# Performance work log

Measured on AMD Instinct MI355X. Metric: run time of the kernel, lower is better.

Reference implementation:

```python
import jax, jax.numpy as jnp
import numpy as np

BS, NA, NE, NAL = 512, 10, 11, 9
H, HEADS, EDIM, ADIM, OWN, NACT, HYP = 64, 4, 8, 8, 14, 17, 64
EOUT = ((EDIM + 1) * H + 1) * HEADS   # 2308: fc1 weights + fc2 attack weights + fc2 attack bias, per head
AOUT = ADIM * H * HEADS               # 2048: ally fc1 weights only (non-MMM map)


def setup_inputs() -> dict:
    key = jax.random.key(0)
    ks = jax.random.split(key, 28)
    N = BS * NA
    s = 0.05
    rn = lambda k, shp: jax.random.normal(k, shp, jnp.float32)
    d = {
        "own_feats": rn(ks[0], (N, OWN)),
        "enemy_feats": rn(ks[1], (N * NE, EDIM)),
        "ally_feats": rn(ks[2], (N * NAL, ADIM)),
        "hidden_state": rn(ks[3], (N, H)),
        "agent_indices": jax.random.randint(ks[4], (N,), 0, NA),
        "last_action_indices": jax.random.randint(ks[5], (N,), 0, NACT),
        "fc1_own_w": rn(ks[6], (H, OWN)) * s,
        "fc1_own_b": rn(ks[7], (H,)) * s,
        "agent_emb": rn(ks[8], (NA, H)) * s,
        "action_emb": rn(ks[9], (NACT, H)) * s,
        "he_w1": rn(ks[10], (HYP, EDIM)) * s,
        "he_b1": rn(ks[11], (HYP,)) * s,
        "he_w2": rn(ks[12], (EOUT, HYP)) * s,
        "he_b2": rn(ks[13], (EOUT,)) * s,
        "ha_w1": rn(ks[14], (HYP, ADIM)) * s,
        "ha_b1": rn(ks[15], (HYP,)) * s,
        "ha_w2": rn(ks[16], (AOUT, HYP)) * s,
        "ha_b2": rn(ks[17], (AOUT,)) * s,
        "merge_in_w": rn(ks[18], (1, HEADS, H)) * s,
        "gru_w_ih": rn(ks[19], (3 * H, H)) * s,
        "gru_w_hh": rn(ks[20], (3 * H, H)) * s,
        "gru_b_ih": rn(ks[21], (3 * H,)) * s,
        "gru_b_hh": rn(ks[22], (3 * H,)) * s,
        "fc2_w": rn(ks[23], (6, H)) * s,
        "fc2_b": rn(ks[24], (6,)) * s,
        "merge_out_w": rn(ks[25], (1, HEADS, 1)) * s,
        "bs": BS,
    }
    return d


def reference(own_feats, enemy_feats, ally_feats, hidden_state, agent_indices,
              last_action_indices, fc1_own_w, fc1_own_b, agent_emb, action_emb,
              he_w1, he_b1, he_w2, he_b2, ha_w1, ha_b1, ha_w2, ha_b2,
              merge_in_w, gru_w_ih, gru_w_hh, gru_b_ih, gru_b_hh,
              fc2_w, fc2_b, merge_out_w, bs):
    N = bs * NA
    cut = (H + 1) * HEADS  # tail of hyper_enemy_out: fc2 attack weights + bias

    # own embedding + id/action embeddings
    emb_own = own_feats @ fc1_own_w.T + fc1_own_b \
        + agent_emb[agent_indices] + action_emb[last_action_indices]

    # enemy hypernet -> per-enemy fc1 weights, then per-entity bmm, sum over enemies
    he_out = jax.nn.relu(enemy_feats @ he_w1.T + he_b1) @ he_w2.T + he_b2  # [N*NE, EOUT]
    fc1_w_e = he_out[:, :-cut].reshape(-1, EDIM, H * HEADS)
    emb_e = jnp.einsum('ne,neh->nh', enemy_feats, fc1_w_e)
    emb_e = emb_e.reshape(N, NE, HEADS, H).sum(axis=1)  # [N, HEADS, H]

    # ally hypernet -> per-ally fc1 weights
    ha_out = jax.nn.relu(ally_feats @ ha_w1.T + ha_b1) @ ha_w2.T + ha_b2  # [N*NAL, AOUT]
    fc1_w_a = ha_out.reshape(-1, ADIM, H * HEADS)
    emb_a = jnp.einsum('na,nah->nh', ally_feats, fc1_w_a)
    emb_a = emb_a.reshape(N, NAL, HEADS, H).sum(axis=1)

    # softmax-weighted multi-head merge + own embedding
    w_in = jax.nn.softmax(merge_in_w, axis=1)  # [1, HEADS, H]
    emb = emb_own + jnp.sum(w_in * (emb_e + emb_a), axis=1)
    x = jax.nn.relu(emb)

    # GRUCell (torch gate order: reset, update, new)
    h_in = hidden_state.reshape(-1, H)
    gi = x @ gru_w_ih.T + gru_b_ih
    gh = h_in @ gru_w_hh.T + gru_b_hh
    i_r, i_z, i_n = jnp.split(gi, 3, axis=1)
    h_r, h_z, h_n = jnp.split(gh, 3, axis=1)
    r = jax.nn.sigmoid(i_r + h_r)
    z = jax.nn.sigmoid(i_z + h_z)
    n = jnp.tanh(i_n + r * h_n)
    hh = (1.0 - z) * n + z * h_in  # [N, H]

    q_normal = (hh @ fc2_w.T + fc2_b).reshape(bs, NA, 6)

    # attack Q values from hypernet-generated fc2
    fc2_w_att = he_out[:, -cut:-HEADS].reshape(N, NE * HEADS, H)
    fc2_b_att = he_out[:, -HEADS:].reshape(N, NE * HEADS)
    q_att = jnp.einsum('nh,nkh->nk', hh, fc2_w_att) + fc2_b_att  # [N, NE*HEADS]
    q_atts = q_att.reshape(N * NE, HEADS, 1)
    w_out = jax.nn.softmax(merge_out_w, axis=1)  # [1, HEADS, 1]
    q_attack = jnp.sum(w_out * q_atts, axis=1).reshape(bs, NA, NE)

    q = jnp.concatenate([q_normal, q_attack], axis=-1)  # [bs, NA, 6+NE]
    return q
```

## Files before the change

### kernel.cpp

```cpp
#include <hip/hip_runtime.h>
#include <hip/hip_bf16.h>
#include <math.h>

#define BS_    512
#define NA_    10
#define NE_    11
#define NAL_   9
#define H_     64
#define HEADS_ 4
#define EDIM_  8
#define ADIM_  8
#define OWN_   14
#define HYP_   64
#define NTOT_  (BS_*NA_)
#define AGB_   8

#define WGRU_US   67584
#define WVV_US    100352
#define WFC2_US   104448
#define WB_OFF    52736
#define B4_OFF    52800
#define FB_OFF    53056
#define WS_FLOATS 53072

typedef __attribute__((ext_vector_type(8))) short short8_t;
typedef __attribute__((ext_vector_type(4))) float f32x4;

__device__ __forceinline__ unsigned short to_bf16(float v) {
    unsigned u = __float_as_uint(v);
    u += 0x7fffu + ((u >> 16) & 1u);
    return (unsigned short)(u >> 16);
}
__device__ __forceinline__ unsigned pack2(float lo, float hi) {
    return ((unsigned)to_bf16(hi) << 16) | to_bf16(lo);
}

__global__ __launch_bounds__(256) void prep_kernel(
    const float* __restrict__ fc1_own_w, const float* __restrict__ fc1_own_b,
    const float* __restrict__ he_w2, const float* __restrict__ he_b2,
    const float* __restrict__ ha_w2, const float* __restrict__ ha_b2,
    const float* __restrict__ merge_in_w,
    const float* __restrict__ gru_w_ih, const float* __restrict__ gru_w_hh,
    const float* __restrict__ gru_b_ih, const float* __restrict__ gru_b_hh,
    const float* __restrict__ merge_out_w,
    const float* __restrict__ fc2_w, const float* __restrict__ fc2_b,
    float* __restrict__ ws)
{
    const int tid = blockIdx.x * blockDim.x + threadIdx.x;

    float wo0, wo1, wo2, wo3;
    {
        float e0 = expf(merge_out_w[0]), e1 = expf(merge_out_w[1]);
        float e2 = expf(merge_out_w[2]), e3 = expf(merge_out_w[3]);
        float inv = 1.0f / (e0 + e1 + e2 + e3);
        wo0 = e0*inv; wo1 = e1*inv; wo2 = e2*inv; wo3 = e3*inv;
    }

    if (tid < 65536) {
        const int half = tid >> 15;
        const int t    = tid & 32767;
        const int col  = t >> 9;
        const int idxL = t & 511;
        const int e    = idxL >> 6;
        const int kk   = idxL & 63;
        const float e0 = expf(merge_in_w[col]),       e1 = expf(merge_in_w[64 + col]);
        const float e2 = expf(merge_in_w[128 + col]), e3 = expf(merge_in_w[192 + col]);
        const float inv = 1.0f / (e0 + e1 + e2 + e3);
        const float wi[4] = { e0*inv, e1*inv, e2*inv, e3*inv };
        const float* Wsrc = half ? ha_w2 : he_w2;
        float v = 0.f;
#pragma unroll
        for (int hd = 0; hd < 4; hd++)
            v += wi[hd] * Wsrc[(size_t)(e*256 + hd*64 + col)*64 + kk];
        const int k   = half*512 + kk*8 + e;
        const int ks  = k >> 5, sub = k & 31;
        const int outp = (col >> 4)*16896 + ks*512 + (((sub >> 3) << 4) + (col & 15))*8 + (sub & 7);
        ((unsigned short*)ws)[outp] = to_bf16(v);
    } else if (tid < 67584) {
        const int t   = tid - 65536;
        const int col = t >> 5;
        const int io  = t & 31;
        float v = 0.f;
        if (io < 16) {
            const float e0 = expf(merge_in_w[col]),       e1 = expf(merge_in_w[64 + col]);
            const float e2 = expf(merge_in_w[128 + col]), e3 = expf(merge_in_w[192 + col]);
            const float inv = 1.0f / (e0 + e1 + e2 + e3);
            const float wi[4] = { e0*inv, e1*inv, e2*inv, e3*inv };
            const float* Bsrc = (io < 8) ? he_b2 : ha_b2;
            const int e = io & 7;
#pragma unroll
            for (int hd = 0; hd < 4; hd++)
                v += wi[hd] * Bsrc[e*256 + hd*64 + col];
        } else if (io < 30) {
            v = fc1_own_w[col*OWN_ + (io - 16)];
        } else if (io == 30) {
            v = fc1_own_b[col];
        }
        const int outp = (col >> 4)*16896 + 32*512 + (((io >> 3) << 4) + (col & 15))*8 + (io & 7);
        ((unsigned short*)ws)[outp] = to_bf16(v);
    } else if (tid < 100352) {
        const int t = tid - 67584;
        const int j  = t & 7;
        const int fl = (t >> 3) & 63;
        const int kstep = (t >> 9) & 3;
        const int T  = t >> 11;
        const int k  = kstep*32 + ((fl >> 4) << 3) + j;
        const int kk = k >> 1;
        const bool hside = (k & 1);
        const int c  = T*16 + (fl & 15);
        const int g  = c >> 6;
        const int u  = c & 63;
        float v;
        if (g == 0)      v = hside ? gru_w_hh[u*64 + kk]       : gru_w_ih[u*64 + kk];
        else if (g == 1) v = hside ? gru_w_hh[(64+u)*64 + kk]  : gru_w_ih[(64+u)*64 + kk];
        else if (g == 2) v = hside ? 0.f                        : gru_w_ih[(128+u)*64 + kk];
        else             v = hside ? gru_w_hh[(128+u)*64 + kk] : 0.f;
        ((unsigned short*)ws)[WGRU_US + t] = to_bf16(v);
    } else if (tid < 104448) {
        const int t = tid - 100352;
        const int j  = t & 7;
        const int fl = (t >> 3) & 63;
        const int kstep = (t >> 9) & 1;
        const int nt = t >> 10;
        const int k  = kstep*32 + ((fl >> 4) << 3) + j;
        const int col = nt*16 + (fl & 15);
        float v = wo0 * he_w2[(2048 + 0*64 + k)*64 + col]
                + wo1 * he_w2[(2048 + 1*64 + k)*64 + col]
                + wo2 * he_w2[(2048 + 2*64 + k)*64 + col]
                + wo3 * he_w2[(2048 + 3*64 + k)*64 + col];
        ((unsigned short*)ws)[WVV_US + t] = to_bf16(v);
    } else if (tid < 105472) {
        const int t = tid - 104448;
        const int j  = t & 7;
        const int fl = (t >> 3) & 63;
        const int kstep = t >> 9;
        const int k  = kstep*32 + ((fl >> 4) << 3) + j;
        const int col = fl & 15;
        float v = 0.f;
        if (col < 6)       v = fc2_w[col*64 + k];
        else if (col == 6) v = wo0*he_b2[2048 + 0*64 + k] + wo1*he_b2[2048 + 1*64 + k]
                             + wo2*he_b2[2048 + 2*64 + k] + wo3*he_b2[2048 + 3*64 + k];
        ((unsigned short*)ws)[WFC2_US + t] = to_bf16(v);
    } else if (tid < 105536) {
        const int k = tid - 105472;
        float v = wo0*he_w2[(2304+0)*64 + k] + wo1*he_w2[(2304+1)*64 + k]
                + wo2*he_w2[(2304+2)*64 + k] + wo3*he_w2[(2304+3)*64 + k];
        ws[WB_OFF + k] = v;
    } else if (tid < 105792) {
        const int c = tid - 105536;
        const int g = c >> 6, u = c & 63;
        float v;
        if (g == 0)      v = gru_b_ih[u]       + gru_b_hh[u];
        else if (g == 1) v = gru_b_ih[64 + u]  + gru_b_hh[64 + u];
        else if (g == 2) v = gru_b_ih[128 + u];
        else             v = gru_b_hh[128 + u];
        ws[B4_OFF + c] = v;
    } else if (tid < 105808) {
        const int col = tid - 105792;
        float v = 0.f;
        if (col < 6)       v = fc2_b[col];
        else if (col == 6) v = wo0*he_b2[2304] + wo1*he_b2[2305] + wo2*he_b2[2306] + wo3*he_b2[2307];
        ws[FB_OFF + col] = v;
    }
}

#define STG_ALLY 704
#define STG_HID  1280
#define STG_OWN  1792

#define AROW_ 1064

__global__ __launch_bounds__(512, 6) void main_kernel(
    const float* __restrict__ own_feats,
    const float* __restrict__ enemy_feats,
    const float* __restrict__ ally_feats,
    const float* __restrict__ hidden_state,
    const int*   __restrict__ agent_idx,
    const int*   __restrict__ last_act,
    const float* __restrict__ agent_emb,
    const float* __restrict__ action_emb,
    const float* __restrict__ he_w1,
    const float* __restrict__ he_b1,
    const float* __restrict__ ha_w1,
    const float* __restrict__ ha_b1,
    const float* __restrict__ ws,
    float* __restrict__ out)
{
    const int tid  = threadIdx.x;
    const int w    = tid >> 6;
    const int lane = tid & 63;
    const int n    = blockIdx.x * AGB_ + w;
    const int q    = w & 3;
    const int kh   = w >> 2;
    const unsigned short* ws_us = (const unsigned short*)ws;

    __shared__ __align__(16) unsigned short a_cmp[AGB_][AROW_];
    __shared__ __align__(16) float scratch[3104];
    float* const stg    = scratch;
    float* const GmF    = scratch;
    float* const pembMF = scratch + 2080;

    {
        const int n0 = blockIdx.x * AGB_;
        const float4* src = nullptr;
        float* dst = nullptr;
        if (tid < 176)      { src = (const float4*)(enemy_feats + (size_t)n0*88) + tid;         dst = stg + tid*4; }
        else if (tid < 320) { src = (const float4*)(ally_feats + (size_t)n0*72) + (tid-176);    dst = stg + STG_ALLY + (tid-176)*4; }
        else if (tid < 448) { src = (const float4*)(hidden_state + (size_t)n0*64) + (tid-320);  dst = stg + STG_HID + (tid-320)*4; }
        else if (tid < 476) { src = (const float4*)(own_feats + (size_t)n0*14) + (tid-448);     dst = stg + STG_OWN + (tid-448)*4; }
        if (src) *(float4*)dst = *src;
    }
    __syncthreads();

    float h_e[NE_];
    float embo, hin_reg;
    {
        const float4 w1a  = *(const float4*)(he_w1 + lane*8);
        const float4 w1b  = *(const float4*)(he_w1 + lane*8 + 4);
        const float  hb1  = he_b1[lane];
        const float* se = stg + w*88;

        float ps[8] = {0,0,0,0,0,0,0,0};
#pragma unroll
        for (int ei = 0; ei < NE_; ei++) {
            const float4 e0 = *(const float4*)(se + ei*8);
            const float4 e1 = *(const float4*)(se + ei*8 + 4);
            float h = hb1;
            h = fmaf(e0.x, w1a.x, h); h = fmaf(e0.y, w1a.y, h);
            h = fmaf(e0.z, w1a.z, h); h = fmaf(e0.w, w1a.w, h);
            h = fmaf(e1.x, w1b.x, h); h = fmaf(e1.y, w1b.y, h);
            h = fmaf(e1.z, w1b.z, h); h = fmaf(e1.w, w1b.w, h);
            h = fmaxf(h, 0.f);
            h_e[ei] = h;
            ps[0] = fmaf(e0.x, h, ps[0]); ps[1] = fmaf(e0.y, h, ps[1]);
            ps[2] = fmaf(e0.z, h, ps[2]); ps[3] = fmaf(e0.w, h, ps[3]);
            ps[4] = fmaf(e1.x, h, ps[4]); ps[5] = fmaf(e1.y, h, ps[5]);
            ps[6] = fmaf(e1.z, h, ps[6]); ps[7] = fmaf(e1.w, h, ps[7]);
        }
        {
            uint4 pk;
            pk.x = pack2(ps[0], ps[1]); pk.y = pack2(ps[2], ps[3]);
            pk.z = pack2(ps[4], ps[5]); pk.w = pack2(ps[6], ps[7]);
            *(uint4*)&a_cmp[w][lane*8] = pk;
        }

        const float4 wa1a = *(const float4*)(ha_w1 + lane*8);
        const float4 wa1b = *(const float4*)(ha_w1 + lane*8 + 4);
        const float  hba1 = ha_b1[lane];
        const float* sa = stg + STG_ALLY + w*72;
        float pa[8] = {0,0,0,0,0,0,0,0};
#pragma unroll
        for (int ai = 0; ai < NAL_; ai++) {
            const float4 a0 = *(const float4*)(sa + ai*8);
            const float4 a1 = *(const float4*)(sa + ai*8 + 4);
            float h = hba1;
            h = fmaf(a0.x, wa1a.x, h); h = fmaf(a0.y, wa1a.y, h);
            h = fmaf(a0.z, wa1a.z, h); h = fmaf(a0.w, wa1a.w, h);
            h = fmaf(a1.x, wa1b.x, h); h = fmaf(a1.y, wa1b.y, h);
            h = fmaf(a1.z, wa1b.z, h); h = fmaf(a1.w, wa1b.w, h);
            h = fmaxf(h, 0.f);
            pa[0] = fmaf(a0.x, h, pa[0]); pa[1] = fmaf(a0.y, h, pa[1]);
            pa[2] = fmaf(a0.z, h, pa[2]); pa[3] = fmaf(a0.w, h, pa[3]);
            pa[4] = fmaf(a1.x, h, pa[4]); pa[5] = fmaf(a1.y, h, pa[5]);
            pa[6] = fmaf(a1.z, h, pa[6]); pa[7] = fmaf(a1.w, h, pa[7]);
        }
        {
            uint4 pk;
            pk.x = pack2(pa[0], pa[1]); pk.y = pack2(pa[2], pa[3]);
            pk.z = pack2(pa[4], pa[5]); pk.w = pack2(pa[6], pa[7]);
            *(uint4*)&a_cmp[w][512 + lane*8] = pk;
        }

        if (lane < 8) {
            float s = 0.f;
            for (int ei = 0; ei < NE_; ei++) s += se[ei*8 + lane];
            a_cmp[w][1024 + lane] = to_bf16(s);
        } else if (lane < 16) {
            const int p = lane - 8;
            float s = 0.f;
            for (int ai = 0; ai < NAL_; ai++) s += sa[ai*8 + p];
            a_cmp[w][1032 + p] = to_bf16(s);
        } else if (lane < 32) {
            float v;
            if (lane < 30)       v = stg[STG_OWN + w*OWN_ + (lane - 16)];
            else if (lane == 30) v = 1.f;
            else                 v = 0.f;
            a_cmp[w][1024 + lane] = to_bf16(v);
        }

        embo = agent_emb[agent_idx[n]*64 + lane] + action_emb[last_act[n]*64 + lane];
        hin_reg = stg[STG_HID + (w << 6) + lane];
    }
    __syncthreads();

    {
        const int ksa = kh ? 17 : 0;
        const int ksb = kh ? 33 : 17;
        f32x4 acc0 = {0.f, 0.f, 0.f, 0.f};
        f32x4 acc1 = {0.f, 0.f, 0.f, 0.f};
        const unsigned short* wpw = ws_us + ((q * 33) << 9);
        const unsigned short* arow = &a_cmp[lane & 7][(lane >> 4) << 3];
        for (int ks = ksa; ks + 1 < ksb; ks += 2) {
            const short8_t a0 = *(const short8_t*)&arow[ks << 5];
            const short8_t b0 = *(const short8_t*)&wpw[(ks << 9) + (lane << 3)];
            acc0 = __builtin_amdgcn_mfma_f32_16x16x32_bf16(a0, b0, acc0, 0, 0, 0);
            const short8_t a1 = *(const short8_t*)&arow[(ks+1) << 5];
            const short8_t b1 = *(const short8_t*)&wpw[((ks+1) << 9) + (lane << 3)];
            acc1 = __builtin_amdgcn_mfma_f32_16x16x32_bf16(a1, b1, acc1, 0, 0, 0);
        }
        if ((ksb - ksa) & 1) {
            const int ks = ksb - 1;
            const short8_t a0 = *(const short8_t*)&arow[ks << 5];
            const short8_t b0 = *(const short8_t*)&wpw[(ks << 9) + (lane << 3)];
            acc0 = __builtin_amdgcn_mfma_f32_16x16x32_bf16(a0, b0, acc0, 0, 0, 0);
        }
        if (lane < 32) {
            const int row = (lane >> 4) * 4;
#pragma unroll
            for (int r = 0; r < 4; ++r)
                pembMF[kh*512 + (row + r)*64 + (q << 4) + (lane & 15)] = acc0[r] + acc1[r];
        }
    }
    __syncthreads();

    {
        const float x = fmaxf(embo + pembMF[w*64 + lane] + pembMF[512 + w*64 + lane], 0.f);
        *(unsigned*)&a_cmp[w][lane*2] = pack2(x, hin_reg);
    }
    __syncthreads();

    {
        short8_t afr[4];
#pragma unroll
        for (int kstep = 0; kstep < 4; ++kstep)
            afr[kstep] = *(const short8_t*)&a_cmp[lane & 7][((lane >> 4) << 3) + (kstep << 5)];

        const unsigned short* wg = ws_us + WGRU_US;
#pragma unroll
        for (int tt = 0; tt < 2; ++tt) {
            const int T = (w << 1) + tt;
            const float b = ws[B4_OFF + (T << 4) + (lane & 15)];
            f32x4 acc = {b, b, b, b};
#pragma unroll
            for (int kstep = 0; kstep < 4; ++kstep) {
                const short8_t bfr = *(const short8_t*)&wg[(((T << 2) + kstep) << 9) + (lane << 3)];
                acc = __builtin_amdgcn_mfma_f32_16x16x32_bf16(afr[kstep], bfr, acc, 0, 0, 0);
            }
            if (lane < 32) {
                const int row = (lane >> 4) * 4;
#pragma unroll
                for (int r = 0; r < 4; ++r) GmF[(row + r)*260 + (T << 4) + (lane & 15)] = acc[r];
            }
        }
    }
    __syncthreads();

    {
        const float gr = GmF[w*260 + lane];
        const float gz = GmF[w*260 + 64 + lane];
        const float gi = GmF[w*260 + 128 + lane];
        const float gh = GmF[w*260 + 192 + lane];
        const float r = 1.f / (1.f + expf(-gr));
        const float z = 1.f / (1.f + expf(-gz));
        const float t = tanhf(gi + r * gh);
        const float hh = (1.f - z) * t + z * hin_reg;
        a_cmp[w][lane] = to_bf16(hh);
    }
    __syncthreads();

    {
        float* vvp = GmF;
        const short8_t av = *(const short8_t*)&a_cmp[lane & 7][((lane >> 4) << 3) + (kh << 5)];
        const short8_t bv = *(const short8_t*)&ws_us[WVV_US + ((((q << 1) + kh) << 9) + (lane << 3))];
        const float wbv = kh ? 0.f : ws[WB_OFF + (q << 4) + (lane & 15)];
        f32x4 acc = {wbv, wbv, wbv, wbv};
        acc = __builtin_amdgcn_mfma_f32_16x16x32_bf16(av, bv, acc, 0, 0, 0);
        if (lane < 32) {
            const int row = (lane >> 4) * 4;
#pragma unroll
            for (int r = 0; r < 4; ++r)
                vvp[kh*512 + (row + r)*64 + (q << 4) + (lane & 15)] = acc[r];
        }
    }
    __syncthreads();

    {
        const float vv = GmF[w*64 + lane] + GmF[512 + w*64 + lane];
        a_cmp[w][64 + lane] = to_bf16(vv);
#pragma unroll
        for (int ei = 0; ei < NE_; ei++)
            a_cmp[w][128 + ei*64 + lane] = to_bf16(h_e[ei]);

        const float fb = ws[FB_OFF + (lane & 15)];
        f32x4 accF = {fb, fb, fb, fb};
        f32x4 accQ = {0.f, 0.f, 0.f, 0.f};
#pragma unroll
        for (int kstep = 0; kstep < 2; ++kstep) {
            const short8_t ah = *(const short8_t*)&a_cmp[lane & 7][((lane >> 4) << 3) + (kstep << 5)];
            const short8_t bf = *(const short8_t*)&ws_us[WFC2_US + (kstep << 9) + (lane << 3)];
            accF = __builtin_amdgcn_mfma_f32_16x16x32_bf16(ah, bf, accF, 0, 0, 0);
            const short8_t aA = *(const short8_t*)&a_cmp[w][128 + (lane & 15)*64 + ((lane >> 4) << 3) + (kstep << 5)];
            const short8_t bV = *(const short8_t*)&a_cmp[w][64 + ((lane >> 4) << 3) + (kstep << 5)];
            accQ = __builtin_amdgcn_mfma_f32_16x16x32_bf16(aA, bV, accQ, 0, 0, 0);
        }

        const int rsel = w & 3;
        float fv = accF[0];
        if (rsel == 1) fv = accF[1];
        else if (rsel == 2) fv = accF[2];
        else if (rsel == 3) fv = accF[3];
        const float sn = __shfl(fv, ((w >> 2) << 4) + 6);

        float* o = out + (size_t)n*17;
        if ((lane >> 4) == (w >> 2) && (lane & 15) < 6)
            o[lane & 15] = fv;
        if ((lane & 15) == 0) {
            const int r0 = (lane >> 4) * 4;
#pragma unroll
            for (int r = 0; r < 4; ++r) {
                const int ei = r0 + r;
                if (ei < NE_) o[6 + ei] = accQ[r] + sn;
            }
        }
    }
}

extern "C" void kernel_launch(void* const* d_in, const int* in_sizes, int n_in,
                              void* d_out, int out_size, void* d_ws, size_t ws_size,
                              hipStream_t stream)
{
    const float* own_feats   = (const float*)d_in[0];
    const float* enemy_feats = (const float*)d_in[1];
    const float* ally_feats  = (const float*)d_in[2];
    const float* hidden      = (const float*)d_in[3];
    const int*   agent_idx   = (const int*)d_in[4];
    const int*   last_act    = (const int*)d_in[5];
    const float* fc1_own_w   = (const float*)d_in[6];
    const float* fc1_own_b   = (const float*)d_in[7];
    const float* agent_emb   = (const float*)d_in[8];
    const float* action_emb  = (const float*)d_in[9];
    const float* he_w1       = (const float*)d_in[10];
    const float* he_b1       = (const float*)d_in[11];
    const float* he_w2       = (const float*)d_in[12];
    const float* he_b2       = (const float*)d_in[13];
    const float* ha_w1       = (const float*)d_in[14];
    const float* ha_b1       = (const float*)d_in[15];
    const float* ha_w2       = (const float*)d_in[16];
    const float* ha_b2       = (const float*)d_in[17];
    const float* merge_in_w  = (const float*)d_in[18];
    const float* gru_w_ih    = (const float*)d_in[19];
    const float* gru_w_hh    = (const float*)d_in[20];
    const float* gru_b_ih    = (const float*)d_in[21];
    const float* gru_b_hh    = (const float*)d_in[22];
    const float* fc2_w       = (const float*)d_in[23];
    const float* fc2_b       = (const float*)d_in[24];
    const float* merge_out_w = (const float*)d_in[25];
    float* out = (float*)d_out;
    float* ws  = (float*)d_ws;

    hipLaunchKernelGGL(prep_kernel, dim3(414), dim3(256), 0, stream,
                       fc1_own_w, fc1_own_b, he_w2, he_b2, ha_w2, ha_b2, merge_in_w,
                       gru_w_ih, gru_w_hh, gru_b_ih, gru_b_hh, merge_out_w,
                       fc2_w, fc2_b, ws);
    hipLaunchKernelGGL(main_kernel, dim3(NTOT_/AGB_), dim3(512), 0, stream,
                       own_feats, enemy_feats, ally_feats, hidden, agent_idx, last_act,
                       agent_emb, action_emb, he_w1, he_b1, ha_w1, ha_b1,
                       ws, out);
}
```

Baseline: 22.72 us.

## Make post-GRU stages per-wave to drop block barriers and LDS round-trips

```diff
diff --git a/kernel.cpp b/kernel.cpp
--- a/kernel.cpp
+++ b/kernel.cpp
@@ -200,6 +200,9 @@
     float* const GmF    = scratch;
     float* const pembMF = scratch + 2080;
 
+    const int ai_r = agent_idx[n];
+    const int la_r = last_act[n];
+
     {
         const int n0 = blockIdx.x * AGB_;
         const float4* src = nullptr;
@@ -288,7 +291,7 @@
             a_cmp[w][1024 + lane] = to_bf16(v);
         }
 
-        embo = agent_emb[agent_idx[n]*64 + lane] + action_emb[last_act[n]*64 + lane];
+        embo = agent_emb[ai_r*64 + lane] + action_emb[la_r*64 + lane];
         hin_reg = stg[STG_HID + (w << 6) + lane];
     }
     __syncthreads();
@@ -365,55 +368,58 @@
         const float t = tanhf(gi + r * gh);
         const float hh = (1.f - z) * t + z * hin_reg;
         a_cmp[w][lane] = to_bf16(hh);
-    }
-    __syncthreads();
-
-    {
-        float* vvp = GmF;
-        const short8_t av = *(const short8_t*)&a_cmp[lane & 7][((lane >> 4) << 3) + (kh << 5)];
-        const short8_t bv = *(const short8_t*)&ws_us[WVV_US + ((((q << 1) + kh) << 9) + (lane << 3))];
-        const float wbv = kh ? 0.f : ws[WB_OFF + (q << 4) + (lane & 15)];
-        f32x4 acc = {wbv, wbv, wbv, wbv};
-        acc = __builtin_amdgcn_mfma_f32_16x16x32_bf16(av, bv, acc, 0, 0, 0);
-        if (lane < 32) {
-            const int row = (lane >> 4) * 4;
-#pragma unroll
-            for (int r = 0; r < 4; ++r)
-                vvp[kh*512 + (row + r)*64 + (q << 4) + (lane & 15)] = acc[r];
-        }
-    }
-    __syncthreads();
-
-    {
-        const float vv = GmF[w*64 + lane] + GmF[512 + w*64 + lane];
-        a_cmp[w][64 + lane] = to_bf16(vv);
 #pragma unroll
         for (int ei = 0; ei < NE_; ei++)
             a_cmp[w][128 + ei*64 + lane] = to_bf16(h_e[ei]);
-
+    }
+
+    {
+        short8_t ah[2];
+#pragma unroll
+        for (int kstep = 0; kstep < 2; ++kstep)
+            ah[kstep] = *(const short8_t*)&a_cmp[w][((lane >> 4) << 3) + (kstep << 5)];
+
+        f32x4 aT0 = {0,0,0,0}, aT1 = {0,0,0,0}, aT2 = {0,0,0,0}, aT3 = {0,0,0,0};
+#pragma unroll
+        for (int kstep = 0; kstep < 2; ++kstep) {
+            const unsigned short* bv = &ws_us[WVV_US + (kstep << 9) + (lane << 3)];
+            aT0 = __builtin_amdgcn_mfma_f32_16x16x32_bf16(ah[kstep], *(const short8_t*)&bv[0 << 10], aT0, 0, 0, 0);
+            aT1 = __builtin_amdgcn_mfma_f32_16x16x32_bf16(ah[kstep], *(const short8_t*)&bv[1 << 10], aT1, 0, 0, 0);
+            aT2 = __builtin_amdgcn_mfma_f32_16x16x32_bf16(ah[kstep], *(const short8_t*)&bv[2 << 10], aT2, 0, 0, 0);
+            aT3 = __builtin_amdgcn_mfma_f32_16x16x32_bf16(ah[kstep], *(const short8_t*)&bv[3 << 10], aT3, 0, 0, 0);
+        }
+        const int nt = lane >> 4;
+        float sel = aT0[0];
+        if (nt == 1) sel = aT1[0];
+        else if (nt == 2) sel = aT2[0];
+        else if (nt == 3) sel = aT3[0];
+        const float vv = sel + ws[WB_OFF + lane];
+        a_cmp[w][64 + lane] = to_bf16(vv);
+    }
+
+    {
+        short8_t ah[2], bVf[2];
+#pragma unroll
+        for (int kstep = 0; kstep < 2; ++kstep) {
+            ah[kstep]  = *(const short8_t*)&a_cmp[w][((lane >> 4) << 3) + (kstep << 5)];
+            bVf[kstep] = *(const short8_t*)&a_cmp[w][64 + ((lane >> 4) << 3) + (kstep << 5)];
+        }
         const float fb = ws[FB_OFF + (lane & 15)];
         f32x4 accF = {fb, fb, fb, fb};
         f32x4 accQ = {0.f, 0.f, 0.f, 0.f};
 #pragma unroll
         for (int kstep = 0; kstep < 2; ++kstep) {
-            const short8_t ah = *(const short8_t*)&a_cmp[lane & 7][((lane >> 4) << 3) + (kstep << 5)];
             const short8_t bf = *(const short8_t*)&ws_us[WFC2_US + (kstep << 9) + (lane << 3)];
-            accF = __builtin_amdgcn_mfma_f32_16x16x32_bf16(ah, bf, accF, 0, 0, 0);
+            accF = __builtin_amdgcn_mfma_f32_16x16x32_bf16(ah[kstep], bf, accF, 0, 0, 0);
             const short8_t aA = *(const short8_t*)&a_cmp[w][128 + (lane & 15)*64 + ((lane >> 4) << 3) + (kstep << 5)];
-            const short8_t bV = *(const short8_t*)&a_cmp[w][64 + ((lane >> 4) << 3) + (kstep << 5)];
-            accQ = __builtin_amdgcn_mfma_f32_16x16x32_bf16(aA, bV, accQ, 0, 0, 0);
-        }
-
-        const int rsel = w & 3;
-        float fv = accF[0];
-        if (rsel == 1) fv = accF[1];
-        else if (rsel == 2) fv = accF[2];
-        else if (rsel == 3) fv = accF[3];
-        const float sn = __shfl(fv, ((w >> 2) << 4) + 6);
+            accQ = __builtin_amdgcn_mfma_f32_16x16x32_bf16(aA, bVf[kstep], accQ, 0, 0, 0);
+        }
+
+        const float fv = accF[0];
+        const float sn = __shfl(fv, 6);
 
         float* o = out + (size_t)n*17;
-        if ((lane >> 4) == (w >> 2) && (lane & 15) < 6)
-            o[lane & 15] = fv;
+        if (lane < 6) o[lane] = fv;
         if ((lane & 15) == 0) {
             const int r0 = (lane >> 4) * 4;
 #pragma unroll
```

Measured after the change: 23.04 us. About the same (+1.4%).

## Process 16 agents per block to fill all MFMA rows, recompute enemy hidden

Applied to the files above, without the earlier changes.

```diff
diff --git a/kernel.cpp b/kernel.cpp
--- a/kernel.cpp
+++ b/kernel.cpp
@@ -13,7 +13,7 @@
 #define OWN_   14
 #define HYP_   64
 #define NTOT_  (BS_*NA_)
-#define AGB_   8
+#define AGB_   16
 
 #define WGRU_US   67584
 #define WVV_US    100352
@@ -164,13 +164,13 @@
     }
 }
 
-#define STG_ALLY 704
-#define STG_HID  1280
-#define STG_OWN  1792
+#define STG_ALLY 1408
+#define STG_HID  2560
+#define STG_OWN  3584
 
 #define AROW_ 1064
 
-__global__ __launch_bounds__(512, 6) void main_kernel(
+__global__ __launch_bounds__(1024, 8) void main_kernel(
     const float* __restrict__ own_feats,
     const float* __restrict__ enemy_feats,
     const float* __restrict__ ally_feats,
@@ -190,29 +190,29 @@
     const int w    = tid >> 6;
     const int lane = tid & 63;
     const int n    = blockIdx.x * AGB_ + w;
-    const int q    = w & 3;
-    const int kh   = w >> 2;
     const unsigned short* ws_us = (const unsigned short*)ws;
 
     __shared__ __align__(16) unsigned short a_cmp[AGB_][AROW_];
-    __shared__ __align__(16) float scratch[3104];
-    float* const stg    = scratch;
-    float* const GmF    = scratch;
-    float* const pembMF = scratch + 2080;
+    __shared__ __align__(16) float scratch[7968];
+    float* const stg = scratch;
+    float* const pm  = scratch + 3808;
+    float* const GmF = scratch + 3808;
+
+    const int ai_r = agent_idx[n];
+    const int la_r = last_act[n];
 
     {
         const int n0 = blockIdx.x * AGB_;
         const float4* src = nullptr;
         float* dst = nullptr;
-        if (tid < 176)      { src = (const float4*)(enemy_feats + (size_t)n0*88) + tid;         dst = stg + tid*4; }
-        else if (tid < 320) { src = (const float4*)(ally_feats + (size_t)n0*72) + (tid-176);    dst = stg + STG_ALLY + (tid-176)*4; }
-        else if (tid < 448) { src = (const float4*)(hidden_state + (size_t)n0*64) + (tid-320);  dst = stg + STG_HID + (tid-320)*4; }
-        else if (tid < 476) { src = (const float4*)(own_feats + (size_t)n0*14) + (tid-448);     dst = stg + STG_OWN + (tid-448)*4; }
+        if (tid < 352)      { src = (const float4*)(enemy_feats + (size_t)n0*88) + tid;         dst = stg + tid*4; }
+        else if (tid < 640) { src = (const float4*)(ally_feats + (size_t)n0*72) + (tid-352);    dst = stg + STG_ALLY + (tid-352)*4; }
+        else if (tid < 896) { src = (const float4*)(hidden_state + (size_t)n0*64) + (tid-640);  dst = stg + STG_HID + (tid-640)*4; }
+        else if (tid < 952) { src = (const float4*)(own_feats + (size_t)n0*14) + (tid-896);     dst = stg + STG_OWN + (tid-896)*4; }
         if (src) *(float4*)dst = *src;
     }
     __syncthreads();
 
-    float h_e[NE_];
     float embo, hin_reg;
     {
         const float4 w1a  = *(const float4*)(he_w1 + lane*8);
@@ -231,7 +231,6 @@
             h = fmaf(e1.x, w1b.x, h); h = fmaf(e1.y, w1b.y, h);
             h = fmaf(e1.z, w1b.z, h); h = fmaf(e1.w, w1b.w, h);
             h = fmaxf(h, 0.f);
-            h_e[ei] = h;
             ps[0] = fmaf(e0.x, h, ps[0]); ps[1] = fmaf(e0.y, h, ps[1]);
             ps[2] = fmaf(e0.z, h, ps[2]); ps[3] = fmaf(e0.w, h, ps[3]);
             ps[4] = fmaf(e1.x, h, ps[4]); ps[5] = fmaf(e1.y, h, ps[5]);
@@ -288,18 +287,20 @@
             a_cmp[w][1024 + lane] = to_bf16(v);
         }
 
-        embo = agent_emb[agent_idx[n]*64 + lane] + action_emb[last_act[n]*64 + lane];
+        embo = agent_emb[ai_r*64 + lane] + action_emb[la_r*64 + lane];
         hin_reg = stg[STG_HID + (w << 6) + lane];
     }
     __syncthreads();
 
     {
-        const int ksa = kh ? 17 : 0;
-        const int ksb = kh ? 33 : 17;
+        const int q  = w & 3;
+        const int kh = w >> 2;
+        const int ksa = kh ? (8*kh + 1) : 0;
+        const int ksb = 8*kh + 9;
         f32x4 acc0 = {0.f, 0.f, 0.f, 0.f};
         f32x4 acc1 = {0.f, 0.f, 0.f, 0.f};
         const unsigned short* wpw = ws_us + ((q * 33) << 9);
-        const unsigned short* arow = &a_cmp[lane & 7][(lane >> 4) << 3];
+        const unsigned short* arow = &a_cmp[lane & 15][(lane >> 4) << 3];
         for (int ks = ksa; ks + 1 < ksb; ks += 2) {
             const short8_t a0 = *(const short8_t*)&arow[ks << 5];
             const short8_t b0 = *(const short8_t*)&wpw[(ks << 9) + (lane << 3)];
@@ -314,17 +315,16 @@
             const short8_t b0 = *(const short8_t*)&wpw[(ks << 9) + (lane << 3)];
             acc0 = __builtin_amdgcn_mfma_f32_16x16x32_bf16(a0, b0, acc0, 0, 0, 0);
         }
-        if (lane < 32) {
-            const int row = (lane >> 4) * 4;
-#pragma unroll
-            for (int r = 0; r < 4; ++r)
-                pembMF[kh*512 + (row + r)*64 + (q << 4) + (lane & 15)] = acc0[r] + acc1[r];
-        }
-    }
-    __syncthreads();
-
-    {
-        const float x = fmaxf(embo + pembMF[w*64 + lane] + pembMF[512 + w*64 + lane], 0.f);
+        const int row = (lane >> 4) * 4;
+#pragma unroll
+        for (int r = 0; r < 4; ++r)
+            pm[kh*1024 + (row + r)*64 + (q << 4) + (lane & 15)] = acc0[r] + acc1[r];
+    }
+    __syncthreads();
+
+    {
+        const float x = fmaxf(embo + pm[w*64 + lane] + pm[1024 + w*64 + lane]
+                                   + pm[2048 + w*64 + lane] + pm[3072 + w*64 + lane], 0.f);
         *(unsigned*)&a_cmp[w][lane*2] = pack2(x, hin_reg);
     }
     __syncthreads();
@@ -333,25 +333,19 @@
         short8_t afr[4];
 #pragma unroll
         for (int kstep = 0; kstep < 4; ++kstep)
-            afr[kstep] = *(const short8_t*)&a_cmp[lane & 7][((lane >> 4) << 3) + (kstep << 5)];
+            afr[kstep] = *(const short8_t*)&a_cmp[lane & 15][((lane >> 4) << 3) + (kstep << 5)];
 
         const unsigned short* wg = ws_us + WGRU_US;
-#pragma unroll
-        for (int tt = 0; tt < 2; ++tt) {
-            const int T = (w << 1) + tt;
-            const float b = ws[B4_OFF + (T << 4) + (lane & 15)];
-            f32x4 acc = {b, b, b, b};
-#pragma unroll
-            for (int kstep = 0; kstep < 4; ++kstep) {
-                const short8_t bfr = *(const short8_t*)&wg[(((T << 2) + kstep) << 9) + (lane << 3)];
-                acc = __builtin_amdgcn_mfma_f32_16x16x32_bf16(afr[kstep], bfr, acc, 0, 0, 0);
-            }
-            if (lane < 32) {
-                const int row = (lane >> 4) * 4;
-#pragma unroll
-                for (int r = 0; r < 4; ++r) GmF[(row + r)*260 + (T << 4) + (lane & 15)] = acc[r];
-            }
-        }
+        const float b = ws[B4_OFF + (w << 4) + (lane & 15)];
+        f32x4 acc = {b, b, b, b};
+#pragma unroll
+        for (int kstep = 0; kstep < 4; ++kstep) {
+            const short8_t bfr = *(const short8_t*)&wg[(((w << 2) + kstep) << 9) + (lane << 3)];
+            acc = __builtin_amdgcn_mfma_f32_16x16x32_bf16(afr[kstep], bfr, acc, 0, 0, 0);
+        }
+        const int row = (lane >> 4) * 4;
+#pragma unroll
+        for (int r = 0; r < 4; ++r) GmF[(row + r)*260 + (w << 4) + (lane & 15)] = acc[r];
     }
     __syncthreads();
 
@@ -368,40 +362,59 @@
     }
     __syncthreads();
 
-    {
+    if (w < 8) {
+        const int q2  = w & 3;
+        const int kh2 = w >> 2;
         float* vvp = GmF;
-        const short8_t av = *(const short8_t*)&a_cmp[lane & 7][((lane >> 4) << 3) + (kh << 5)];
-        const short8_t bv = *(const short8_t*)&ws_us[WVV_US + ((((q << 1) + kh) << 9) + (lane << 3))];
-        const float wbv = kh ? 0.f : ws[WB_OFF + (q << 4) + (lane & 15)];
+        const short8_t av = *(const short8_t*)&a_cmp[lane & 15][((lane >> 4) << 3) + (kh2 << 5)];
+        const short8_t bv = *(const short8_t*)&ws_us[WVV_US + ((((q2 << 1) + kh2) << 9) + (lane << 3))];
+        const float wbv = kh2 ? 0.f : ws[WB_OFF + (q2 << 4) + (lane & 15)];
         f32x4 acc = {wbv, wbv, wbv, wbv};
         acc = __builtin_amdgcn_mfma_f32_16x16x32_bf16(av, bv, acc, 0, 0, 0);
-        if (lane < 32) {
-            const int row = (lane >> 4) * 4;
-#pragma unroll
-            for (int r = 0; r < 4; ++r)
-                vvp[kh*512 + (row + r)*64 + (q << 4) + (lane & 15)] = acc[r];
-        }
-    }
-    __syncthreads();
-
-    {
-        const float vv = GmF[w*64 + lane] + GmF[512 + w*64 + lane];
+        const int row = (lane >> 4) * 4;
+#pragma unroll
+        for (int r = 0; r < 4; ++r)
+            vvp[kh2*1024 + (row + r)*64 + (q2 << 4) + (lane & 15)] = acc[r];
+    }
+    __syncthreads();
+
+    {
+        const float vv = GmF[w*64 + lane] + GmF[1024 + w*64 + lane];
         a_cmp[w][64 + lane] = to_bf16(vv);
-#pragma unroll
-        for (int ei = 0; ei < NE_; ei++)
-            a_cmp[w][128 + ei*64 + lane] = to_bf16(h_e[ei]);
-
+
+        {
+            const float4 w1a = *(const float4*)(he_w1 + lane*8);
+            const float4 w1b = *(const float4*)(he_w1 + lane*8 + 4);
+            const float  hb1 = he_b1[lane];
+            const float* se  = stg + w*88;
+#pragma unroll
+            for (int ei = 0; ei < NE_; ei++) {
+                const float4 e0 = *(const float4*)(se + ei*8);
+                const float4 e1 = *(const float4*)(se + ei*8 + 4);
+                float h = hb1;
+                h = fmaf(e0.x, w1a.x, h); h = fmaf(e0.y, w1a.y, h);
+                h = fmaf(e0.z, w1a.z, h); h = fmaf(e0.w, w1a.w, h);
+                h = fmaf(e1.x, w1b.x, h); h = fmaf(e1.y, w1b.y, h);
+                h = fmaf(e1.z, w1b.z, h); h = fmaf(e1.w, w1b.w, h);
+                a_cmp[w][128 + ei*64 + lane] = to_bf16(fmaxf(h, 0.f));
+            }
+        }
+
+        short8_t ah[2], bVf[2];
+#pragma unroll
+        for (int kstep = 0; kstep < 2; ++kstep) {
+            ah[kstep]  = *(const short8_t*)&a_cmp[lane & 15][((lane >> 4) << 3) + (kstep << 5)];
+            bVf[kstep] = *(const short8_t*)&a_cmp[w][64 + ((lane >> 4) << 3) + (kstep << 5)];
+        }
         const float fb = ws[FB_OFF + (lane & 15)];
         f32x4 accF = {fb, fb, fb, fb};
         f32x4 accQ = {0.f, 0.f, 0.f, 0.f};
 #pragma unroll
         for (int kstep = 0; kstep < 2; ++kstep) {
-            const short8_t ah = *(const short8_t*)&a_cmp[lane & 7][((lane >> 4) << 3) + (kstep << 5)];
             const short8_t bf = *(const short8_t*)&ws_us[WFC2_US + (kstep << 9) + (lane << 3)];
-            accF = __builtin_amdgcn_mfma_f32_16x16x32_bf16(ah, bf, accF, 0, 0, 0);
+            accF = __builtin_amdgcn_mfma_f32_16x16x32_bf16(ah[kstep], bf, accF, 0, 0, 0);
             const short8_t aA = *(const short8_t*)&a_cmp[w][128 + (lane & 15)*64 + ((lane >> 4) << 3) + (kstep << 5)];
-            const short8_t bV = *(const short8_t*)&a_cmp[w][64 + ((lane >> 4) << 3) + (kstep << 5)];
-            accQ = __builtin_amdgcn_mfma_f32_16x16x32_bf16(aA, bV, accQ, 0, 0, 0);
+            accQ = __builtin_amdgcn_mfma_f32_16x16x32_bf16(aA, bVf[kstep], accQ, 0, 0, 0);
         }
 
         const int rsel = w & 3;
@@ -462,7 +475,7 @@
                        fc1_own_w, fc1_own_b, he_w2, he_b2, ha_w2, ha_b2, merge_in_w,
                        gru_w_ih, gru_w_hh, gru_b_ih, gru_b_hh, merge_out_w,
                        fc2_w, fc2_b, ws);
-    hipLaunchKernelGGL(main_kernel, dim3(NTOT_/AGB_), dim3(512), 0, stream,
+    hipLaunchKernelGGL(main_kernel, dim3(NTOT_/AGB_), dim3(1024), 0, stream,
                        own_feats, enemy_feats, ally_feats, hidden, agent_idx, last_act,
                        agent_emb, action_emb, he_w1, he_b1, ha_w1, ha_b1,
                        ws, out);
```

Result: slower. 26.80 us (+18.0%).
